# Performance work log

Measured on AMD Instinct MI355X. Metric: run time of the kernel, lower is better.

The kernel has to match this reference:

```python
import jax, jax.numpy as jnp
import numpy as np

B, C, T = 16, 512, 2048
C8 = C // 8

def setup_inputs() -> dict:
    key = jax.random.key(0)
    ks = jax.random.split(key, 8)
    s = 0.05
    return {
        "x": jax.random.normal(ks[0], (B, C, T), dtype=jnp.float32),
        "wq": jax.random.normal(ks[1], (C8, C), dtype=jnp.float32) * s,
        "bq": jax.random.normal(ks[2], (C8,), dtype=jnp.float32) * s,
        "wk": jax.random.normal(ks[3], (C8, C), dtype=jnp.float32) * s,
        "bk": jax.random.normal(ks[4], (C8,), dtype=jnp.float32) * s,
        "wv": jax.random.normal(ks[5], (C, C), dtype=jnp.float32) * s,
        "bv": jax.random.normal(ks[6], (C,), dtype=jnp.float32) * s,
        "gamma": jax.random.normal(ks[7], (1,), dtype=jnp.float32),
    }

def reference(x, wq, bq, wk, bk, wv, bv, gamma):
    # conv1x1 == channel-wise linear: (out_ch, in_ch) @ (B, in_ch, T)
    q = jnp.einsum('dc,bct->bdt', wq, x) + bq[None, :, None]   # (B, C8, T)
    k = jnp.einsum('dc,bct->bdt', wk, x) + bk[None, :, None]   # (B, C8, T)
    v = jnp.einsum('oc,bct->bot', wv, x) + bv[None, :, None]   # (B, C, T)
    # attn[b,t,s] = sum_d q[b,d,t] * k[b,d,s]; softmax over s (no scaling, as in source)
    attn = jax.nn.softmax(jnp.einsum('bdt,bds->bts', q, k), axis=-1)  # (B, T, T)
    out = jnp.einsum('bcs,bts->bct', v, attn)                  # (B, C, T)
    return gamma * out + x
```

## Files before the change

### kernel.cpp

```cpp
#include <hip/hip_runtime.h>
#include <hip/hip_bf16.h>
#include <math.h>

#define B_N 16
#define C_N 512
#define T_N 2048
#define D_N 64
#define LOG2E 1.44269504088896340736f

typedef __attribute__((ext_vector_type(4))) float f32x4;
typedef __attribute__((ext_vector_type(8))) __bf16 bf16x8;
typedef __attribute__((ext_vector_type(8))) unsigned short us8;
typedef __attribute__((ext_vector_type(4))) unsigned short us4;

__device__ inline f32x4 mfma16(bf16x8 a, bf16x8 b, f32x4 c) {
    return __builtin_amdgcn_mfma_f32_16x16x32_bf16(a, b, c, 0, 0, 0);
}
__device__ inline unsigned short f2bf_bits(float v) {
    return __builtin_bit_cast(unsigned short, __float2bfloat16(v));
}
__device__ inline float bfbits2f(unsigned short u) {
    unsigned int x = ((unsigned int)u) << 16;
    return __builtin_bit_cast(float, x);
}

#define QIDX(t,d) (((((t)<<6) | (d))) ^ ((((t)&7))<<3))
#define KIDX(s,d) (((((s)<<6) | (d))) ^ ((((s)&7))<<3))
#define VIDX2(c,s) (((c)<<5) | ((s) ^ (((((c)>>1))&3)<<3)))
#define PIDX(t,s) (((((t)<<5) | (s))) ^ ((((t)&7))<<3))

#define GLD_LDS(src, dst) \
    __builtin_amdgcn_global_load_lds( \
        (const __attribute__((address_space(1))) void*)(src), \
        (__attribute__((address_space(3))) void*)(dst), 16, 0, 0)

__global__ __launch_bounds__(256) void convert_kernel(
    const float* __restrict__ x,
    const float* __restrict__ wq, const float* __restrict__ wk,
    const float* __restrict__ wv,
    unsigned short* __restrict__ xt, unsigned short* __restrict__ whb)
{
    const int blk = blockIdx.x;
    const int tid = threadIdx.x;

    if (blk < 4096) {
        const int b  = blk >> 8;
        const int rem = blk & 255;
        const int c0 = (rem >> 5) << 6;
        const int t0 = (rem & 31) << 6;

        __shared__ float Xs[64][65];
        const int lt = tid & 63, lc0 = tid >> 6;
        #pragma unroll
        for (int r = 0; r < 16; ++r)
            Xs[lc0 + r * 4][lt] =
                x[((size_t)b * C_N + c0 + lc0 + r * 4) * T_N + t0 + lt];
        __syncthreads();
        #pragma unroll
        for (int k = 0; k < 2; ++k) {
            const int j = tid + k * 256;
            const int tr = j >> 3, sg = j & 7;
            us8 v;
            #pragma unroll
            for (int e = 0; e < 8; ++e)
                v[e] = f2bf_bits(Xs[sg * 8 + e][tr]);
            *(us8*)&xt[((size_t)b * T_N + t0 + tr) * C_N + c0 + sg * 8] = v;
        }
    } else {
        const int wi = blk - 4096;
        #pragma unroll
        for (int q = 0; q < 8; ++q) {
            const int idx4 = wi * 8192 + q * 1024 + tid * 4;
            const float* s; int off;
            if (idx4 < 32768)      { s = wq; off = idx4; }
            else if (idx4 < 65536) { s = wk; off = idx4 - 32768; }
            else                   { s = wv; off = idx4 - 65536; }
            const float4 v4 = *(const float4*)&s[off];
            us4 h;
            h[0] = f2bf_bits(v4.x); h[1] = f2bf_bits(v4.y);
            h[2] = f2bf_bits(v4.z); h[3] = f2bf_bits(v4.w);
            *(us4*)&whb[idx4] = h;
        }
    }
}

__global__ __launch_bounds__(512, 3) void qkv_mfma_kernel(
    const unsigned short* __restrict__ xt, const unsigned short* __restrict__ whb,
    const float* __restrict__ bq, const float* __restrict__ bk,
    const float* __restrict__ bv,
    unsigned short* __restrict__ qth, unsigned short* __restrict__ qtl,
    unsigned short* __restrict__ kth, unsigned short* __restrict__ ktl,
    unsigned short* __restrict__ vh)
{
    __shared__ unsigned short XTs[2][8192];
    __shared__ unsigned short Ws[2][4096];

    const int tid  = threadIdx.x;
    const int wave = tid >> 6;
    const int lane = tid & 63;
    const int ln   = lane & 15;
    const int lg   = lane >> 4;

    const int l    = blockIdx.x;
    const int low3 = l & 7;
    const int rest = l >> 3;
    const int ob   = rest % 10;
    const int ph   = rest / 10;
    const int pair = (ph << 3) | low3;
    const int b    = pair >> 4;
    const int t0   = (pair & 15) << 7;

    const unsigned short* wbase; const float* bias; int orow0;
    if (ob == 0)      { wbase = whb;          bias = bq; orow0 = 0; }
    else if (ob == 1) { wbase = whb + 32768;  bias = bk; orow0 = 0; }
    else              { wbase = whb + 65536;  bias = bv; orow0 = (ob - 2) * 64; }

    const unsigned short* xb = xt + (size_t)b * T_N * C_N;

    const int wo = wave & 3;
    const int wt = wave >> 2;

    auto DMA = [&](int it, int buf) {
        const int c0 = it * 64;
        #pragma unroll
        for (int k = 0; k < 2; ++k) {
            const int j = tid + k * 512;
            const int t = j >> 3, cs = j & 7;
            const unsigned short* src =
                xb + (size_t)(t0 + t) * C_N + c0 + ((cs ^ (t & 7)) << 3);
            GLD_LDS(src, &XTs[buf][j * 8]);
        }
        {
            const int o = tid >> 3, cs = tid & 7;
            const unsigned short* src =
                wbase + (size_t)(orow0 + o) * C_N + c0 + ((cs ^ (o & 7)) << 3);
            if (tid < 512) GLD_LDS(src, &Ws[buf][tid * 8]);
        }
    };

    f32x4 acc[4];
    #pragma unroll
    for (int st = 0; st < 4; ++st) acc[st] = (f32x4){0.f, 0.f, 0.f, 0.f};

    DMA(0, 0);

    int p = 0;
    for (int it = 0; it < 8; ++it) {
        asm volatile("s_waitcnt vmcnt(0)" ::: "memory");
        __builtin_amdgcn_sched_barrier(0);
        __builtin_amdgcn_s_barrier();
        __builtin_amdgcn_sched_barrier(0);

        if (it < 7) DMA(it + 1, p ^ 1);

        #pragma unroll
        for (int kk = 0; kk < 2; ++kk) {
            const int co = kk * 32 + lg * 8;
            const bf16x8 ah = __builtin_bit_cast(bf16x8,
                *(const us8*)&Ws[p][(((wo * 16 + ln) << 6) | co) ^ ((ln & 7) << 3)]);
            #pragma unroll
            for (int st = 0; st < 4; ++st) {
                const int t = wt * 64 + st * 16 + ln;
                const bf16x8 bv8 = __builtin_bit_cast(bf16x8,
                    *(const us8*)&XTs[p][((t << 6) | co) ^ ((ln & 7) << 3)]);
                acc[st] = mfma16(ah, bv8, acc[st]);
            }
        }
        p ^= 1;
    }

    __syncthreads();

    float bb[4];
    #pragma unroll
    for (int r = 0; r < 4; ++r) bb[r] = bias[orow0 + wo * 16 + lg * 4 + r];

    unsigned short* ep0 = &XTs[0][0];
    unsigned short* ep1 = &XTs[1][0];

    if (ob < 2) {
        #pragma unroll
        for (int st = 0; st < 4; ++st) {
            const int t = wt * 64 + st * 16 + ln;
            #pragma unroll
            for (int r = 0; r < 4; ++r) {
                const float v = acc[st][r] + bb[r];
                const int o = wo * 16 + lg * 4 + r;
                const int idx = ((t << 6) | o) ^ ((t & 7) << 3);
                const unsigned short hb = f2bf_bits(v);
                ep0[idx] = hb;
                ep1[idx] = f2bf_bits(v - bfbits2f(hb));
            }
        }
        __syncthreads();
        unsigned short* dh = (ob == 0) ? qth : kth;
        unsigned short* dl = (ob == 0) ? qtl : ktl;
        #pragma unroll
        for (int k = 0; k < 2; ++k) {
            const int j = tid + k * 512;
            const int t = j >> 3, sg = j & 7;
            const int idx = (t << 6) | ((sg ^ (t & 7)) << 3);
            const size_t off = ((size_t)b * T_N + t0 + t) * 64 + sg * 8;
            *(us8*)&dh[off] = *(const us8*)&ep0[idx];
            *(us8*)&dl[off] = *(const us8*)&ep1[idx];
        }
    } else {
        #pragma unroll
        for (int st = 0; st < 4; ++st) {
            const int t = wt * 64 + st * 16 + ln;
            #pragma unroll
            for (int r = 0; r < 4; ++r) {
                const int o = wo * 16 + lg * 4 + r;
                const int idx = ((o << 7) | t) ^ ((o & 7) << 3);
                ep0[idx] = f2bf_bits(acc[st][r] + bb[r]);
            }
        }
        __syncthreads();
        #pragma unroll
        for (int k = 0; k < 2; ++k) {
            const int j = tid + k * 512;
            const int o = j >> 4, sg = j & 15;
            const int idx = ((o << 7) | (sg << 3)) ^ ((o & 7) << 3);
            const size_t off = ((size_t)b * C_N + orow0 + o) * T_N + t0 + sg * 8;
            *(us8*)&vh[off] = *(const us8*)&ep0[idx];
        }
    }
}

__global__ __launch_bounds__(512, 4) void attn_mfma_kernel(
    const float* __restrict__ x,
    const unsigned short* __restrict__ qth, const unsigned short* __restrict__ qtl,
    const unsigned short* __restrict__ kth, const unsigned short* __restrict__ ktl,
    const unsigned short* __restrict__ vh,
    const float* __restrict__ gamma,
    float* __restrict__ out)
{
    __shared__ unsigned short Qh_s[64 * 64];
    __shared__ unsigned short Ql_s[64 * 64];
    __shared__ unsigned short Kh_s[2][32 * 64];
    __shared__ unsigned short Kl_s[2][32 * 64];
    __shared__ unsigned short V_s[512 * 32];
    __shared__ unsigned short P_s[8 * 16 * 32];

    const int tid  = threadIdx.x;
    const int wave = tid >> 6;
    const int lane = tid & 63;
    const int ln   = lane & 15;
    const int lg   = lane >> 4;

    const int l    = blockIdx.x;
    const int slot = l >> 3;
    const int b    = ((l & 7) << 1) | (slot & 1);
    const int t0   = (slot >> 1) * 64;

    const int tb = wave & 3;
    const int ch = wave >> 2;

    const unsigned short* kb_h = kth + (size_t)b * T_N * 64;
    const unsigned short* kb_l = ktl + (size_t)b * T_N * 64;
    const unsigned short* vb   = vh  + (size_t)b * C_N * T_N;

    auto DMA_K = [&](int s0, int buf) {
        const int w4   = wave & 3;
        const int chnk = w4 * 64 + lane;
        const int s    = chnk >> 3, jl = chnk & 7;
        const unsigned short* src =
            ((wave < 4) ? kb_h : kb_l) + (((size_t)(s0 + s)) << 6) + ((jl ^ (s & 7)) << 3);
        unsigned short* dst = ((wave < 4) ? &Kh_s[buf][0] : &Kl_s[buf][0]) + w4 * 512;
        GLD_LDS(src, dst);
    };
    auto DMA_V = [&](int s0) {
        #pragma unroll
        for (int q = 0; q < 4; ++q) {
            const int chnk = wave * 256 + q * 64 + lane;
            const int c = chnk >> 2, kl = chnk & 3;
            const int ks = kl ^ ((c >> 1) & 3);
            const unsigned short* src = vb + (size_t)c * T_N + s0 + ks * 8;
            unsigned short* dst = &V_s[0] + (wave * 256 + q * 64) * 8;
            GLD_LDS(src, dst);
        }
    };

    {
        const int r = tid >> 3, c8 = (tid & 7) * 8;
        const size_t off = ((size_t)b * T_N + t0 + r) * 64 + c8;
        const int idx = QIDX(r, c8);
        *(us8*)&Qh_s[idx] = *(const us8*)&qth[off];
        *(us8*)&Ql_s[idx] = *(const us8*)&qtl[off];
    }
    DMA_K(0, 0);
    asm volatile("s_waitcnt lgkmcnt(0)" ::: "memory");
    __builtin_amdgcn_sched_barrier(0);

    const int trow = tb * 16 + ln;

    float m_run[4], l_run[4];
    #pragma unroll
    for (int r = 0; r < 4; ++r) { m_run[r] = -INFINITY; l_run[r] = 0.f; }

    f32x4 acc[16];
    #pragma unroll
    for (int ct = 0; ct < 16; ++ct) acc[ct] = (f32x4){0.f, 0.f, 0.f, 0.f};

    int p = 0;
    for (int it = 0; it < 64; ++it) {
        const int s0 = it * 32;

        asm volatile("s_waitcnt vmcnt(0)" ::: "memory");
        __builtin_amdgcn_sched_barrier(0);
        __builtin_amdgcn_s_barrier();
        __builtin_amdgcn_sched_barrier(0);

        DMA_V(s0);
        const int nx = (it + 1 < 64 ? it + 1 : 63) * 32;
        DMA_K(nx, p ^ 1);

        const unsigned short* khp = &Kh_s[p][0];
        const unsigned short* klp = &Kl_s[p][0];

        f32x4 S[2];
        S[0] = (f32x4){0.f, 0.f, 0.f, 0.f};
        S[1] = (f32x4){0.f, 0.f, 0.f, 0.f};
        #pragma unroll
        for (int kk = 0; kk < 2; ++kk) {
            const int d0 = kk * 32 + lg * 8;
            const bf16x8 ah = __builtin_bit_cast(bf16x8, *(const us8*)&Qh_s[QIDX(trow, d0)]);
            const bf16x8 al = __builtin_bit_cast(bf16x8, *(const us8*)&Ql_s[QIDX(trow, d0)]);
            #pragma unroll
            for (int st = 0; st < 2; ++st) {
                const int srow = st * 16 + ln;
                const bf16x8 bh = __builtin_bit_cast(bf16x8, *(const us8*)&khp[KIDX(srow, d0)]);
                const bf16x8 bl = __builtin_bit_cast(bf16x8, *(const us8*)&klp[KIDX(srow, d0)]);
                S[st] = mfma16(ah, bh, S[st]);
                S[st] = mfma16(ah, bl, S[st]);
                S[st] = mfma16(al, bh, S[st]);
            }
        }

        float rs[4];
        #pragma unroll
        for (int r = 0; r < 4; ++r) {
            float mx = fmaxf(S[0][r], S[1][r]);
            mx = fmaxf(mx, __shfl_xor(mx, 1));
            mx = fmaxf(mx, __shfl_xor(mx, 2));
            mx = fmaxf(mx, __shfl_xor(mx, 4));
            mx = fmaxf(mx, __shfl_xor(mx, 8));
            const float m_new = fmaxf(m_run[r], mx);
            const float rr = exp2f((m_run[r] - m_new) * LOG2E);
            const float p0 = exp2f((S[0][r] - m_new) * LOG2E);
            const float p1 = exp2f((S[1][r] - m_new) * LOG2E);
            float sm = p0 + p1;
            sm += __shfl_xor(sm, 1);
            sm += __shfl_xor(sm, 2);
            sm += __shfl_xor(sm, 4);
            sm += __shfl_xor(sm, 8);
            l_run[r] = l_run[r] * rr + sm;
            m_run[r] = m_new;
            rs[r] = rr;
            const int t = lg * 4 + r;
            P_s[wave * 512 + PIDX(t, ln)]      = f2bf_bits(p0);
            P_s[wave * 512 + PIDX(t, 16 + ln)] = f2bf_bits(p1);
        }

        #pragma unroll
        for (int ct = 0; ct < 16; ++ct)
            #pragma unroll
            for (int r = 0; r < 4; ++r) acc[ct][r] *= rs[r];

        asm volatile("s_waitcnt vmcnt(1)" ::: "memory");
        __builtin_amdgcn_sched_barrier(0);
        __builtin_amdgcn_s_barrier();
        __builtin_amdgcn_sched_barrier(0);

        const bf16x8 pa = __builtin_bit_cast(bf16x8,
            *(const us8*)&P_s[wave * 512 + PIDX(ln, lg * 8)]);
        #pragma unroll
        for (int ct = 0; ct < 16; ++ct) {
            const int c = ch * 256 + ct * 16 + ln;
            const bf16x8 bv = __builtin_bit_cast(bf16x8, *(const us8*)&V_s[VIDX2(c, lg * 8)]);
            acc[ct] = mfma16(pa, bv, acc[ct]);
        }
        p ^= 1;
    }

    const float g = gamma[0];
    float invl[4];
    #pragma unroll
    for (int r = 0; r < 4; ++r) invl[r] = 1.0f / l_run[r];

    const float* xb = x + (size_t)b * C_N * T_N;
    float* ob_ = out + (size_t)b * C_N * T_N;
    const int tl0 = t0 + tb * 16 + lg * 4;

    #pragma unroll
    for (int ct = 0; ct < 16; ++ct) {
        const int c = ch * 256 + ct * 16 + ln;
        const size_t off = (size_t)c * T_N + tl0;
        const float4 xv = *(const float4*)&xb[off];
        float4 o4;
        o4.x = g * acc[ct][0] * invl[0] + xv.x;
        o4.y = g * acc[ct][1] * invl[1] + xv.y;
        o4.z = g * acc[ct][2] * invl[2] + xv.z;
        o4.w = g * acc[ct][3] * invl[3] + xv.w;
        *(float4*)&ob_[off] = o4;
    }
}

extern "C" void kernel_launch(void* const* d_in, const int* in_sizes, int n_in,
                              void* d_out, int out_size, void* d_ws, size_t ws_size,
                              hipStream_t stream)
{
    const float* x     = (const float*)d_in[0];
    const float* wq    = (const float*)d_in[1];
    const float* bq    = (const float*)d_in[2];
    const float* wk    = (const float*)d_in[3];
    const float* bk    = (const float*)d_in[4];
    const float* wv    = (const float*)d_in[5];
    const float* bv    = (const float*)d_in[6];
    const float* gamma = (const float*)d_in[7];
    float* out = (float*)d_out;

    unsigned short* qth = (unsigned short*)d_ws;
    unsigned short* qtl = qth + (size_t)B_N * T_N * 64;
    unsigned short* kth = qtl + (size_t)B_N * T_N * 64;
    unsigned short* ktl = kth + (size_t)B_N * T_N * 64;
    unsigned short* vh  = ktl + (size_t)B_N * T_N * 64;
    unsigned short* xt  = vh  + (size_t)B_N * C_N * T_N;
    unsigned short* whb = xt  + (size_t)B_N * T_N * C_N;

    convert_kernel<<<4136, 256, 0, stream>>>(x, wq, wk, wv, xt, whb);

    qkv_mfma_kernel<<<2560, 512, 0, stream>>>(xt, whb, bq, bk, bv,
                                              qth, qtl, kth, ktl, vh);

    attn_mfma_kernel<<<512, 512, 0, stream>>>(x, qth, qtl, kth, ktl, vh, gamma, out);

    (void)in_sizes; (void)n_in; (void)out_size; (void)ws_size;
}
```

Measured before the change: 465.2 us.

## Split QK/softmax onto four waves, use 32x32 MFMA for PV with lazy rescale

Only four waves now compute the QK^T scores and softmax. They write P and per-row rescale factors to shared memory, and all eight waves then do the PV product with 32x32x16 bf16 MFMAs over 32-row by 128-channel tiles. The running max is only updated when the new max exceeds the old one by more than 8, so the accumulator rescale is skipped in most iterations. This removes duplicated QK work and rescale multiplies and gives larger MFMA tiles. In exchange it adds LDS traffic for P and the scale factors, leaves four waves idle during the score phase, and risks larger exp values because the stored max can lag the true max.

```diff
diff --git a/kernel.cpp b/kernel.cpp
--- a/kernel.cpp
+++ b/kernel.cpp
@@ -9,12 +9,16 @@
 #define LOG2E 1.44269504088896340736f
 
 typedef __attribute__((ext_vector_type(4))) float f32x4;
+typedef __attribute__((ext_vector_type(16))) float f32x16;
 typedef __attribute__((ext_vector_type(8))) __bf16 bf16x8;
 typedef __attribute__((ext_vector_type(8))) unsigned short us8;
 typedef __attribute__((ext_vector_type(4))) unsigned short us4;
 
 __device__ inline f32x4 mfma16(bf16x8 a, bf16x8 b, f32x4 c) {
     return __builtin_amdgcn_mfma_f32_16x16x32_bf16(a, b, c, 0, 0, 0);
+}
+__device__ inline f32x16 mfma32(bf16x8 a, bf16x8 b, f32x16 c) {
+    return __builtin_amdgcn_mfma_f32_32x32x16_bf16(a, b, c, 0, 0, 0);
 }
 __device__ inline unsigned short f2bf_bits(float v) {
     return __builtin_bit_cast(unsigned short, __float2bfloat16(v));
@@ -240,13 +244,18 @@
     __shared__ unsigned short Kh_s[2][32 * 64];
     __shared__ unsigned short Kl_s[2][32 * 64];
     __shared__ unsigned short V_s[512 * 32];
-    __shared__ unsigned short P_s[8 * 16 * 32];
+    __shared__ unsigned short P2[64 * 32];
+    __shared__ float r_lds[64];
+    __shared__ float l_lds[64];
+    __shared__ unsigned nflag[4];
 
     const int tid  = threadIdx.x;
     const int wave = tid >> 6;
     const int lane = tid & 63;
     const int ln   = lane & 15;
     const int lg   = lane >> 4;
+    const int hi   = lane >> 5;
+    const int l31  = lane & 31;
 
     const int l    = blockIdx.x;
     const int slot = l >> 3;
@@ -254,7 +263,8 @@
     const int t0   = (slot >> 1) * 64;
 
     const int tb = wave & 3;
-    const int ch = wave >> 2;
+    const int tq = wave & 1;
+    const int cq = wave >> 1;
 
     const unsigned short* kb_h = kth + (size_t)b * T_N * 64;
     const unsigned short* kb_l = ktl + (size_t)b * T_N * 64;
@@ -298,9 +308,11 @@
     #pragma unroll
     for (int r = 0; r < 4; ++r) { m_run[r] = -INFINITY; l_run[r] = 0.f; }
 
-    f32x4 acc[16];
+    f32x16 acc32[4];
     #pragma unroll
-    for (int ct = 0; ct < 16; ++ct) acc[ct] = (f32x4){0.f, 0.f, 0.f, 0.f};
+    for (int ci = 0; ci < 4; ++ci)
+        #pragma unroll
+        for (int j = 0; j < 16; ++j) acc32[ci][j] = 0.f;
 
     int p = 0;
     for (int it = 0; it < 64; ++it) {
@@ -315,94 +327,151 @@
         const int nx = (it + 1 < 64 ? it + 1 : 63) * 32;
         DMA_K(nx, p ^ 1);
 
-        const unsigned short* khp = &Kh_s[p][0];
-        const unsigned short* klp = &Kl_s[p][0];
-
-        f32x4 S[2];
-        S[0] = (f32x4){0.f, 0.f, 0.f, 0.f};
-        S[1] = (f32x4){0.f, 0.f, 0.f, 0.f};
-        #pragma unroll
-        for (int kk = 0; kk < 2; ++kk) {
-            const int d0 = kk * 32 + lg * 8;
-            const bf16x8 ah = __builtin_bit_cast(bf16x8, *(const us8*)&Qh_s[QIDX(trow, d0)]);
-            const bf16x8 al = __builtin_bit_cast(bf16x8, *(const us8*)&Ql_s[QIDX(trow, d0)]);
-            #pragma unroll
-            for (int st = 0; st < 2; ++st) {
-                const int srow = st * 16 + ln;
-                const bf16x8 bh = __builtin_bit_cast(bf16x8, *(const us8*)&khp[KIDX(srow, d0)]);
-                const bf16x8 bl = __builtin_bit_cast(bf16x8, *(const us8*)&klp[KIDX(srow, d0)]);
-                S[st] = mfma16(ah, bh, S[st]);
-                S[st] = mfma16(ah, bl, S[st]);
-                S[st] = mfma16(al, bh, S[st]);
-            }
-        }
-
-        float rs[4];
-        #pragma unroll
-        for (int r = 0; r < 4; ++r) {
-            float mx = fmaxf(S[0][r], S[1][r]);
-            mx = fmaxf(mx, __shfl_xor(mx, 1));
-            mx = fmaxf(mx, __shfl_xor(mx, 2));
-            mx = fmaxf(mx, __shfl_xor(mx, 4));
-            mx = fmaxf(mx, __shfl_xor(mx, 8));
-            const float m_new = fmaxf(m_run[r], mx);
-            const float rr = exp2f((m_run[r] - m_new) * LOG2E);
-            const float p0 = exp2f((S[0][r] - m_new) * LOG2E);
-            const float p1 = exp2f((S[1][r] - m_new) * LOG2E);
-            float sm = p0 + p1;
-            sm += __shfl_xor(sm, 1);
-            sm += __shfl_xor(sm, 2);
-            sm += __shfl_xor(sm, 4);
-            sm += __shfl_xor(sm, 8);
-            l_run[r] = l_run[r] * rr + sm;
-            m_run[r] = m_new;
-            rs[r] = rr;
-            const int t = lg * 4 + r;
-            P_s[wave * 512 + PIDX(t, ln)]      = f2bf_bits(p0);
-            P_s[wave * 512 + PIDX(t, 16 + ln)] = f2bf_bits(p1);
-        }
-
-        #pragma unroll
-        for (int ct = 0; ct < 16; ++ct)
-            #pragma unroll
-            for (int r = 0; r < 4; ++r) acc[ct][r] *= rs[r];
-
-        asm volatile("s_waitcnt vmcnt(1)" ::: "memory");
+        if (wave < 4) {
+            const unsigned short* khp = &Kh_s[p][0];
+            const unsigned short* klp = &Kl_s[p][0];
+
+            f32x4 S[2];
+            S[0] = (f32x4){0.f, 0.f, 0.f, 0.f};
+            S[1] = (f32x4){0.f, 0.f, 0.f, 0.f};
+            __builtin_amdgcn_s_setprio(1);
+            #pragma unroll
+            for (int kk = 0; kk < 2; ++kk) {
+                const int d0 = kk * 32 + lg * 8;
+                const bf16x8 ah = __builtin_bit_cast(bf16x8, *(const us8*)&Qh_s[QIDX(trow, d0)]);
+                const bf16x8 al = __builtin_bit_cast(bf16x8, *(const us8*)&Ql_s[QIDX(trow, d0)]);
+                #pragma unroll
+                for (int st = 0; st < 2; ++st) {
+                    const int srow = st * 16 + ln;
+                    const bf16x8 bh = __builtin_bit_cast(bf16x8, *(const us8*)&khp[KIDX(srow, d0)]);
+                    const bf16x8 bl = __builtin_bit_cast(bf16x8, *(const us8*)&klp[KIDX(srow, d0)]);
+                    S[st] = mfma16(ah, bh, S[st]);
+                    S[st] = mfma16(ah, bl, S[st]);
+                    S[st] = mfma16(al, bh, S[st]);
+                }
+            }
+            __builtin_amdgcn_s_setprio(0);
+
+            float mx[4];
+            #pragma unroll
+            for (int r = 0; r < 4; ++r) {
+                float m = fmaxf(S[0][r], S[1][r]);
+                m = fmaxf(m, __shfl_xor(m, 1));
+                m = fmaxf(m, __shfl_xor(m, 2));
+                m = fmaxf(m, __shfl_xor(m, 4));
+                m = fmaxf(m, __shfl_xor(m, 8));
+                mx[r] = m;
+            }
+            int needl = 0;
+            #pragma unroll
+            for (int r = 0; r < 4; ++r) needl |= (mx[r] > m_run[r] + 8.0f);
+            const int need = __any(needl);
+
+            float rr[4];
+            if (need) {
+                #pragma unroll
+                for (int r = 0; r < 4; ++r) {
+                    const float m_new = fmaxf(m_run[r], mx[r]);
+                    rr[r] = exp2f((m_run[r] - m_new) * LOG2E);
+                    m_run[r] = m_new;
+                }
+            } else {
+                #pragma unroll
+                for (int r = 0; r < 4; ++r) rr[r] = 1.0f;
+            }
+
+            #pragma unroll
+            for (int r = 0; r < 4; ++r) {
+                const float p0 = exp2f((S[0][r] - m_run[r]) * LOG2E);
+                const float p1 = exp2f((S[1][r] - m_run[r]) * LOG2E);
+                float sm = p0 + p1;
+                sm += __shfl_xor(sm, 1);
+                sm += __shfl_xor(sm, 2);
+                sm += __shfl_xor(sm, 4);
+                sm += __shfl_xor(sm, 8);
+                l_run[r] = l_run[r] * rr[r] + sm;
+                const int t = tb * 16 + lg * 4 + r;
+                P2[PIDX(t, ln)]      = f2bf_bits(p0);
+                P2[PIDX(t, 16 + ln)] = f2bf_bits(p1);
+            }
+            if (ln == 0) {
+                #pragma unroll
+                for (int r = 0; r < 4; ++r)
+                    r_lds[tb * 16 + lg * 4 + r] = rr[r];
+            }
+            if (lane == 0) nflag[tb] = need ? 1u : 0u;
+        }
+
+        asm volatile("s_waitcnt vmcnt(1) lgkmcnt(0)" ::: "memory");
         __builtin_amdgcn_sched_barrier(0);
         __builtin_amdgcn_s_barrier();
         __builtin_amdgcn_sched_barrier(0);
 
-        const bf16x8 pa = __builtin_bit_cast(bf16x8,
-            *(const us8*)&P_s[wave * 512 + PIDX(ln, lg * 8)]);
-        #pragma unroll
-        for (int ct = 0; ct < 16; ++ct) {
-            const int c = ch * 256 + ct * 16 + ln;
-            const bf16x8 bv = __builtin_bit_cast(bf16x8, *(const us8*)&V_s[VIDX2(c, lg * 8)]);
-            acc[ct] = mfma16(pa, bv, acc[ct]);
-        }
+        const unsigned f = nflag[0] | nflag[1] | nflag[2] | nflag[3];
+        if (f) {
+            float4 rq[4];
+            #pragma unroll
+            for (int q = 0; q < 4; ++q)
+                rq[q] = *(const float4*)&r_lds[tq * 32 + 8 * q + 4 * hi];
+            #pragma unroll
+            for (int ci = 0; ci < 4; ++ci)
+                #pragma unroll
+                for (int j = 0; j < 16; ++j)
+                    acc32[ci][j] *= ((const float*)&rq[j >> 2])[j & 3];
+        }
+
+        __builtin_amdgcn_s_setprio(1);
+        #pragma unroll
+        for (int sk = 0; sk < 2; ++sk) {
+            const bf16x8 pa = __builtin_bit_cast(bf16x8,
+                *(const us8*)&P2[PIDX(tq * 32 + l31, sk * 16 + hi * 8)]);
+            #pragma unroll
+            for (int ci = 0; ci < 4; ++ci) {
+                const int c = cq * 128 + ci * 32 + l31;
+                const bf16x8 bv = __builtin_bit_cast(bf16x8,
+                    *(const us8*)&V_s[VIDX2(c, sk * 16 + hi * 8)]);
+                acc32[ci] = mfma32(pa, bv, acc32[ci]);
+            }
+        }
+        __builtin_amdgcn_s_setprio(0);
         p ^= 1;
     }
 
+    if (wave < 4 && ln == 0) {
+        #pragma unroll
+        for (int r = 0; r < 4; ++r)
+            l_lds[tb * 16 + lg * 4 + r] = l_run[r];
+    }
+    __syncthreads();
+
     const float g = gamma[0];
-    float invl[4];
+    float4 il[4];
     #pragma unroll
-    for (int r = 0; r < 4; ++r) invl[r] = 1.0f / l_run[r];
+    for (int q = 0; q < 4; ++q) {
+        const float4 lv = *(const float4*)&l_lds[tq * 32 + 8 * q + 4 * hi];
+        il[q].x = 1.0f / lv.x; il[q].y = 1.0f / lv.y;
+        il[q].z = 1.0f / lv.z; il[q].w = 1.0f / lv.w;
+    }
 
     const float* xb = x + (size_t)b * C_N * T_N;
     float* ob_ = out + (size_t)b * C_N * T_N;
-    const int tl0 = t0 + tb * 16 + lg * 4;
 
     #pragma unroll
-    for (int ct = 0; ct < 16; ++ct) {
-        const int c = ch * 256 + ct * 16 + ln;
-        const size_t off = (size_t)c * T_N + tl0;
-        const float4 xv = *(const float4*)&xb[off];
-        float4 o4;
-        o4.x = g * acc[ct][0] * invl[0] + xv.x;
-        o4.y = g * acc[ct][1] * invl[1] + xv.y;
-        o4.z = g * acc[ct][2] * invl[2] + xv.z;
-        o4.w = g * acc[ct][3] * invl[3] + xv.w;
-        *(float4*)&ob_[off] = o4;
+    for (int ci = 0; ci < 4; ++ci) {
+        const int c = cq * 128 + ci * 32 + l31;
+        const size_t base = (size_t)c * T_N + t0 + tq * 32 + 4 * hi;
+        #pragma unroll
+        for (int q = 0; q < 4; ++q) {
+            const size_t off = base + 8 * q;
+            const float4 xv = *(const float4*)&xb[off];
+            const float* ilq = (const float*)&il[q];
+            float4 o4;
+            o4.x = g * acc32[ci][4 * q + 0] * ilq[0] + xv.x;
+            o4.y = g * acc32[ci][4 * q + 1] * ilq[1] + xv.y;
+            o4.z = g * acc32[ci][4 * q + 2] * ilq[2] + xv.z;
+            o4.w = g * acc32[ci][4 * q + 3] * ilq[3] + xv.w;
+            *(float4*)&ob_[off] = o4;
+        }
     }
 }
 
```

After: 443.3 us. 4.7% less time.
